# Kernel optimization log

Hardware: AMD Instinct MI355X
Metric: run time of the kernel (lower is better)

The kernel has to match this reference:

```python
import jax, jax.numpy as jnp
import numpy as np

N = 4096      # nodes
F_IN = 512    # nfeat
D = 64        # nhid per head
H = 8         # nheads
C = 16        # nclass
K = 2         # k hops
ALPHA = 0.2   # leakyrelu slope
BETA = 0.9    # hop decay
NEG = jnp.float32(-9e15)


def _lrelu(v):
    return jnp.where(v > 0, v, ALPHA * v)


def setup_inputs() -> dict:
    key = jax.random.key(0)
    ks = jax.random.split(key, 8)
    x = jax.random.normal(ks[0], (N, F_IN), jnp.float32)
    # k-hop neighbor masks (dense, sparse-ish occupancy); self-loops kept so no row is fully masked
    masks = jax.random.bernoulli(ks[1], 0.01, (K, N, N))
    masks = masks | jnp.eye(N, dtype=bool)[None]
    W = jax.random.normal(ks[2], (H, F_IN, D), jnp.float32) * 0.05
    a1 = jax.random.normal(ks[3], (H, D), jnp.float32) * 0.05
    a2 = jax.random.normal(ks[4], (H, D), jnp.float32) * 0.05
    W_out = jax.random.normal(ks[5], (H * D, C), jnp.float32) * 0.05
    a_out1 = jax.random.normal(ks[6], (C,), jnp.float32) * 0.05
    a_out2 = jax.random.normal(ks[7], (C,), jnp.float32) * 0.05
    return dict(x=x, masks=masks, W=W, a1=a1, a2=a2, W_out=W_out, a_out1=a_out1, a_out2=a_out2)


def reference(x, masks, W, a1, a2, W_out, a_out1, a_out2):
    # ---- multi-head k-hop GAT layers (concat=True) ----
    Wh = jnp.einsum('nf,hfd->hnd', x, W)                      # [H,N,D]
    f1 = jnp.einsum('hnd,hd->hn', Wh, a1)                     # source term
    f2 = jnp.einsum('hnd,hd->hn', Wh, a2)                     # target term
    e = _lrelu(f1[:, :, None] + f2[:, None, :])               # [H,N,N]
    h = jnp.zeros_like(Wh)
    for hop in range(K):                                      # fixed small k
        att = jax.nn.softmax(jnp.where(masks[hop][None], e, NEG), axis=-1)
        h = h + (BETA ** hop) * jnp.einsum('hnm,hmd->hnd', att, Wh)
    h = jax.nn.elu(h)                                         # concat=True applies elu
    x2 = jnp.transpose(h, (1, 0, 2)).reshape(N, H * D)        # head concat

    # ---- output k-hop attention layer (concat=False) ----
    Who = x2 @ W_out                                          # [N,C]
    e2 = _lrelu((Who @ a_out1)[:, None] + (Who @ a_out2)[None, :])  # [N,N]
    out = jnp.zeros_like(Who)
    for hop in range(K):
        att = jax.nn.softmax(jnp.where(masks[hop], e2, NEG), axis=-1)
        out = out + (BETA ** hop) * (att @ Who)
    out = jax.nn.elu(out)
    return jax.nn.log_softmax(out, axis=1)
```

## Files before the change

kernel.cpp:

```cpp
#include <hip/hip_runtime.h>
#include <cstdint>

#define NN 4096
#define FIN 512
#define DD 64
#define HH 8
#define CC 16
#define KHOP 2
#define ALPHA 0.2f
#define BETA 0.9f

typedef __attribute__((ext_vector_type(8))) short short8;
typedef __attribute__((ext_vector_type(4))) float floatx4;

static __device__ __forceinline__ uint16_t f2bf(float f) {
    uint32_t u = __float_as_uint(f);
    u += 0x7FFFu + ((u >> 16) & 1u);
    return (uint16_t)(u >> 16);
}

static __device__ __forceinline__ uint32_t nz_nib(uint32_t x) {
    uint32_t zero80 = (x - 0x01010101u) & ~x & 0x80808080u;
    uint32_t nz80 = zero80 ^ 0x80808080u;
    return ((nz80 >> 7) * 0x01020408u) >> 24;
}

__global__ __launch_bounds__(256) void bits_prep(const uint32_t* __restrict__ mraw,
                                                 uint64_t* __restrict__ bits,
                                                 const float* __restrict__ W,
                                                 uint16_t* __restrict__ Wt) {
    const int tid = threadIdx.x;
    if (blockIdx.x >= 1024) {
        const int b = blockIdx.x - 1024;
        const int h = b >> 3, kt = b & 7;
        __shared__ float tile[64][65];
        {
            const int kr = tid >> 4, d4 = (tid & 15) * 4;
#pragma unroll
            for (int r = 0; r < 4; ++r) {
                const int k = kr + r * 16;
                float4 v = *(const float4*)&W[((size_t)h * FIN + kt * 64 + k) * DD + d4];
                tile[k][d4 + 0] = v.x; tile[k][d4 + 1] = v.y;
                tile[k][d4 + 2] = v.z; tile[k][d4 + 3] = v.w;
            }
        }
        __syncthreads();
        const int d = tid >> 2, kb = (tid & 3) * 16;
        uint16_t tmp[16];
#pragma unroll
        for (int i = 0; i < 16; ++i) tmp[i] = f2bf(tile[kb + i][d]);
        uint4 o0, o1;
        o0.x = tmp[0] | ((uint32_t)tmp[1] << 16);  o0.y = tmp[2] | ((uint32_t)tmp[3] << 16);
        o0.z = tmp[4] | ((uint32_t)tmp[5] << 16);  o0.w = tmp[6] | ((uint32_t)tmp[7] << 16);
        o1.x = tmp[8] | ((uint32_t)tmp[9] << 16);  o1.y = tmp[10] | ((uint32_t)tmp[11] << 16);
        o1.z = tmp[12] | ((uint32_t)tmp[13] << 16); o1.w = tmp[14] | ((uint32_t)tmp[15] << 16);
        uint16_t* dst = Wt + ((size_t)h * DD + d) * FIN + kt * 64 + kb;
        *(uint4*)dst = o0;
        *(uint4*)(dst + 8) = o1;
        return;
    }
    const int totalWords = KHOP * NN * (NN / 64);
    __shared__ int sflag;
    if (tid == 0) sflag = 1;
    __syncthreads();
    bool ok = true;
    for (int i = tid; i < 4096; i += 256) {
        uint32_t w = mraw[i];
        if (!(w == 0u || w == 1u || w == 0x3F800000u)) ok = false;
    }
    if (!ok) sflag = 0;
    __syncthreads();
    const int flag = sflag;

    const int wave_id = (blockIdx.x * 256 + tid) >> 6;
    const int lane = tid & 63;

    if (!flag) {
        const uint8_t* m8 = (const uint8_t*)mraw;
        const uint8_t* base = m8 + (size_t)wave_id * 8192 + (size_t)lane * 16;
        uint4 v[8];
#pragma unroll
        for (int i = 0; i < 8; ++i)
            v[i] = *(const uint4*)(base + (size_t)i * 1024);
        const int idx = (lane & 15) * 4;
#pragma unroll
        for (int i = 0; i < 8; ++i) {
            uint32_t m16 = nz_nib(v[i].x) | (nz_nib(v[i].y) << 4) |
                           (nz_nib(v[i].z) << 8) | (nz_nib(v[i].w) << 12);
            uint32_t u0 = (uint32_t)__shfl((int)m16, idx);
            uint32_t u1 = (uint32_t)__shfl((int)m16, idx + 1);
            uint32_t u2 = (uint32_t)__shfl((int)m16, idx + 2);
            uint32_t u3 = (uint32_t)__shfl((int)m16, idx + 3);
            if (lane < 16) {
                uint64_t wrd = (uint64_t)((u0 & 0xFFFFu) | (u1 << 16)) |
                               ((uint64_t)((u2 & 0xFFFFu) | (u3 << 16)) << 32);
                bits[(size_t)wave_id * 128 + i * 16 + lane] = wrd;
            }
        }
    } else {
        const int w0b = wave_id * 128;
        for (int w0 = w0b; w0 < w0b + 128 && w0 < totalWords; w0 += 8) {
            uint32_t v[8];
#pragma unroll
            for (int i = 0; i < 8; ++i)
                v[i] = mraw[(size_t)(w0 + i) * 64 + lane];
#pragma unroll
            for (int i = 0; i < 8; ++i) {
                unsigned long long b = __ballot(v[i] != 0u);
                if (lane == 0) bits[w0 + i] = b;
            }
        }
    }
}

__global__ __launch_bounds__(256) void wh_gemm(const float* __restrict__ x,
                                               const uint16_t* __restrict__ Wt,
                                               const float* __restrict__ a1,
                                               const float* __restrict__ a2,
                                               uint16_t* __restrict__ Whb,
                                               float* __restrict__ f1,
                                               float* __restrict__ f2) {
    const int h = blockIdx.y;
    const int n0 = blockIdx.x * 64;
    const int tid = threadIdx.x;
    const int wave = tid >> 6, lane = tid & 63;
    const int q = lane >> 4, r = lane & 15;
    __shared__ uint16_t xs[64 * 72];
    __shared__ uint16_t ws[64 * 72];
    floatx4 acc[4] = {floatx4{0,0,0,0}, floatx4{0,0,0,0}, floatx4{0,0,0,0}, floatx4{0,0,0,0}};

    for (int chunk = 0; chunk < 8; ++chunk) {
        const int fc = chunk * 64;
        {
            const int row = tid >> 4, c4 = (tid & 15) * 4;
#pragma unroll
            for (int rr = 0; rr < 4; ++rr) {
                const int n = row + rr * 16;
                float4 v = *(const float4*)&x[(size_t)(n0 + n) * FIN + fc + c4];
                ushort4 o;
                o.x = f2bf(v.x); o.y = f2bf(v.y); o.z = f2bf(v.z); o.w = f2bf(v.w);
                *(ushort4*)&xs[n * 72 + c4] = o;
            }
            const int d = tid >> 2, kb = (tid & 3) * 16;
            const uint16_t* src = Wt + ((size_t)h * DD + d) * FIN + fc + kb;
            uint4 w0 = *(const uint4*)src;
            uint4 w1 = *(const uint4*)(src + 8);
            *(uint4*)&ws[d * 72 + kb] = w0;
            *(uint4*)&ws[d * 72 + kb + 8] = w1;
        }
        __syncthreads();
        const int mrow = wave * 16 + r;
        short8 a0 = *(const short8*)&xs[mrow * 72 + q * 8];
        short8 a1f = *(const short8*)&xs[mrow * 72 + 32 + q * 8];
#pragma unroll
        for (int t = 0; t < 4; ++t) {
            short8 b0 = *(const short8*)&ws[(t * 16 + r) * 72 + q * 8];
            short8 b1 = *(const short8*)&ws[(t * 16 + r) * 72 + 32 + q * 8];
            acc[t] = __builtin_amdgcn_mfma_f32_16x16x32_bf16(a0, b0, acc[t], 0, 0, 0);
            acc[t] = __builtin_amdgcn_mfma_f32_16x16x32_bf16(a1f, b1, acc[t], 0, 0, 0);
        }
        __syncthreads();
    }

#pragma unroll
    for (int t = 0; t < 4; ++t) {
#pragma unroll
        for (int reg = 0; reg < 4; ++reg) {
            const int m = wave * 16 + q * 4 + reg;
            const int d = t * 16 + r;
            Whb[((size_t)h * NN + n0 + m) * DD + d] = f2bf(acc[t][reg]);
        }
    }
    float a1r[4], a2r[4];
#pragma unroll
    for (int t = 0; t < 4; ++t) {
        a1r[t] = a1[h * DD + t * 16 + r];
        a2r[t] = a2[h * DD + t * 16 + r];
    }
#pragma unroll
    for (int reg = 0; reg < 4; ++reg) {
        float p1 = 0.f, p2 = 0.f;
#pragma unroll
        for (int t = 0; t < 4; ++t) {
            p1 += acc[t][reg] * a1r[t];
            p2 += acc[t][reg] * a2r[t];
        }
#pragma unroll
        for (int off = 1; off < 16; off <<= 1) {
            p1 += __shfl_xor(p1, off);
            p2 += __shfl_xor(p2, off);
        }
        if (r == 0) {
            const int m = wave * 16 + q * 4 + reg;
            f1[h * NN + n0 + m] = p1;
            f2[h * NN + n0 + m] = p2;
        }
    }
}

__global__ __launch_bounds__(512) void attn1(const uint64_t* __restrict__ bits,
                                             const uint16_t* __restrict__ Whb,
                                             const float* __restrict__ f1,
                                             const float* __restrict__ f2,
                                             const float* __restrict__ Wout,
                                             const float* __restrict__ ao1,
                                             const float* __restrict__ ao2,
                                             float* __restrict__ Who,
                                             float* __restrict__ g1,
                                             float* __restrict__ g2) {
    const int n = blockIdx.x;
    const int tid = threadIdx.x;
    const int h = tid >> 6, lane = tid & 63;
    const int hl = lane & 31, uh = lane >> 5;
    __shared__ uint16_t nbr[KHOP][NN];
    __shared__ uint2 wm[HH][64];
    __shared__ float xrow[HH * DD];
    __shared__ float part[32][17];
    __shared__ int cnt[KHOP];
    if (h < KHOP) {
        const int hop = h;
        if (lane == 0) cnt[hop] = 0;
        uint64_t v = bits[((size_t)hop * NN + n) * 64 + lane];
        int c = __popcll(v);
        int base = 0;
        if (c) base = atomicAdd(&cnt[hop], c);
        int mb = lane * 64;
        while (v) {
            int j = __ffsll((unsigned long long)v) - 1;
            nbr[hop][base++] = (uint16_t)(mb + j);
            v &= v - 1;
        }
    }
    const float f1n = f1[h * NN + n];
    const float* __restrict__ f2h = f2 + h * NN;
    const uint16_t* __restrict__ hb = Whb + (size_t)h * NN * DD;
    const uint32_t dbyte = (uint32_t)hl * 4;
    __syncthreads();
    float res0 = 0.f, res1 = 0.f;
    for (int hop = 0; hop < KHOP; ++hop) {
        const int count = cnt[hop];
        const uint16_t* __restrict__ nb = nbr[hop];
        uint2* __restrict__ wmh = wm[h];
        float acc0 = 0.f, acc1 = 0.f, denp = 0.f;
        for (int b0 = 0; b0 < count; b0 += 64) {
            const int bs = min(64, count - b0);
            uint32_t wbits = 0u, moff = 0u;
            if (lane < bs) {
                int m = nb[b0 + lane];
                float e = f1n + f2h[m];
                e = (e > 0.f) ? e : ALPHA * e;
                float w = __expf(e);
                denp += w;
                wbits = __float_as_uint(w);
                moff = (uint32_t)m << 7;
            }
            wmh[lane] = make_uint2(wbits, moff);
            const int npair8 = ((((bs + 1) >> 1) + 7) & ~7);
            for (int c0 = 0; c0 < npair8; c0 += 8) {
                uint2 pw[8];
#pragma unroll
                for (int i = 0; i < 8; ++i)
                    pw[i] = wmh[2 * (c0 + i) + uh];
#pragma unroll
                for (int i = 0; i < 8; ++i) {
                    const uint32_t dv =
                        *(const uint32_t*)((const char*)hb + (pw[i].y + dbyte));
                    const float w = __uint_as_float(pw[i].x);
                    acc0 += w * __uint_as_float(dv << 16);
                    acc1 += w * __uint_as_float(dv & 0xFFFF0000u);
                }
            }
        }
        float den = denp;
#pragma unroll
        for (int off = 1; off < 64; off <<= 1) den += __shfl_xor(den, off);
        acc0 += __shfl_xor(acc0, 32);
        acc1 += __shfl_xor(acc1, 32);
        const float scale = ((hop == 0) ? 1.f : BETA) / den;
        res0 += scale * acc0;
        res1 += scale * acc1;
    }
    float v0 = (res0 > 0.f) ? res0 : (__expf(res0) - 1.f);
    float v1 = (res1 > 0.f) ? res1 : (__expf(res1) - 1.f);
    if (uh == 0) {
        xrow[h * DD + 2 * hl]     = v0;
        xrow[h * DD + 2 * hl + 1] = v1;
    }
    __syncthreads();
    {
        const int c = tid & 15, chunk = tid >> 4;
        float p = 0.f;
#pragma unroll
        for (int i = 0; i < 16; ++i)
            p += xrow[chunk * 16 + i] * Wout[(chunk * 16 + i) * CC + c];
        part[chunk][c] = p;
    }
    __syncthreads();
    if (tid < 16) {
        float s = 0.f;
#pragma unroll
        for (int k = 0; k < 32; ++k) s += part[k][tid];
        Who[n * CC + tid] = s;
        float p1 = s * ao1[tid];
        float p2 = s * ao2[tid];
#pragma unroll
        for (int off = 1; off < 16; off <<= 1) {
            p1 += __shfl_xor(p1, off);
            p2 += __shfl_xor(p2, off);
        }
        if (tid == 0) { g1[n] = p1; g2[n] = p2; }
    }
}

__global__ __launch_bounds__(256) void attn2(const uint64_t* __restrict__ bits,
                                             const float* __restrict__ Who,
                                             const float* __restrict__ g1,
                                             const float* __restrict__ g2,
                                             float* __restrict__ out) {
    const int wv = threadIdx.x >> 6;
    const int lane = threadIdx.x & 63;
    const int n = blockIdx.x * 4 + wv;
    __shared__ uint16_t nbr[4][NN];
    uint16_t* mynbr = nbr[wv];
    const float g1n = g1[n];
    const int c = lane & 15, s = lane >> 4;
    const uint32_t cbyte = (uint32_t)c * 4;
    float res = 0.f;
    for (int hop = 0; hop < KHOP; ++hop) {
        uint64_t v = bits[((size_t)hop * NN + n) * 64 + lane];
        int cpc = __popcll(v);
        int pref = cpc;
        for (int off = 1; off < 64; off <<= 1) {
            int t = __shfl_up(pref, off);
            if (lane >= off) pref += t;
        }
        int total = __shfl(pref, 63);
        int base = pref - cpc;
        int mb = lane * 64;
        while (v) {
            int j = __ffsll((unsigned long long)v) - 1;
            mynbr[base++] = (uint16_t)(mb + j);
            v &= v - 1;
        }
        float acc = 0.f, denp = 0.f;
        for (int b0 = 0; b0 < total; b0 += 64) {
            const int bs = min(64, total - b0);
            float w = 0.f; uint32_t moff = 0u;
            if (lane < bs) {
                int m = mynbr[b0 + lane];
                float e = g1n + g2[m];
                e = (e > 0.f) ? e : ALPHA * e;
                w = __expf(e);
                moff = (uint32_t)m << 6;
            }
            denp += w;
            const int nit = (((bs + 3) >> 2) + 1) & ~1;
#pragma unroll 2
            for (int i = 0; i < nit; ++i) {
                const int j = 4 * i + s;
                const float wj = __shfl(w, j);
                const uint32_t oj = (uint32_t)__shfl((int)moff, j);
                const float v2 = *(const float*)((const char*)Who + (oj + cbyte));
                acc += wj * v2;
            }
        }
        float den = denp;
#pragma unroll
        for (int off = 1; off < 64; off <<= 1) den += __shfl_xor(den, off);
        acc += __shfl_xor(acc, 16);
        acc += __shfl_xor(acc, 32);
        res += ((hop == 0) ? 1.f : BETA) * (acc / den);
    }
    float o = (res > 0.f) ? res : (__expf(res) - 1.f);
    float mx = o;
    for (int off = 1; off < 16; off <<= 1) mx = fmaxf(mx, __shfl_xor(mx, off));
    float ex = __expf(o - mx);
    float sum = ex;
    for (int off = 1; off < 16; off <<= 1) sum += __shfl_xor(sum, off);
    float r = o - mx - __logf(sum);
    if (lane < 16) out[n * CC + c] = r;
}

extern "C" void kernel_launch(void* const* d_in, const int* in_sizes, int n_in,
                              void* d_out, int out_size, void* d_ws, size_t ws_size,
                              hipStream_t stream) {
    const float* x    = (const float*)d_in[0];
    const void*  masks= d_in[1];
    const float* W    = (const float*)d_in[2];
    const float* a1   = (const float*)d_in[3];
    const float* a2   = (const float*)d_in[4];
    const float* Wout = (const float*)d_in[5];
    const float* ao1  = (const float*)d_in[6];
    const float* ao2  = (const float*)d_in[7];
    float* out = (float*)d_out;

    char* ws = (char*)d_ws;
    uint64_t* bits = (uint64_t*)ws;
    uint16_t* Whb  = (uint16_t*)(ws + (size_t)KHOP * NN * 64 * 8);
    float* f1  = (float*)(Whb + (size_t)HH * NN * DD);
    float* f2  = f1 + (size_t)HH * NN;
    float* Who = f2 + (size_t)HH * NN;
    float* g1  = Who + (size_t)NN * CC;
    float* g2  = g1 + NN;
    uint16_t* Wt = (uint16_t*)(g2 + NN);

    bits_prep<<<1024 + HH * (FIN / 64), 256, 0, stream>>>((const uint32_t*)masks, bits, W, Wt);
    wh_gemm<<<dim3(NN / 64, HH), 256, 0, stream>>>(x, Wt, a1, a2, Whb, f1, f2);
    attn1<<<NN, 512, 0, stream>>>(bits, Whb, f1, f2, Wout, ao1, ao2, Who, g1, g2);
    attn2<<<NN / 4, 256, 0, stream>>>(bits, Who, g1, g2, out);
    (void)in_sizes; (void)n_in; (void)out_size; (void)ws_size;
}
```

Measured before the change: 280.6 us.

## Pre-convert x to bf16 once and widen gather loads in attention kernels

Adds extra blocks to the prep kernel that convert x to bf16 once, so wh_gemm no longer re-reads and converts fp32 x for each of the 8 heads. attn1 now has each lane load 16 bytes (8 bf16 features) per neighbor, with 8 neighbors processed in parallel per wave, instead of 4-byte loads. attn2 likewise switches to float4 gathers with 16 neighbors per step. This cuts redundant global traffic and load instruction count, at the cost of more register use and a larger cross-lane reduction.

```diff
diff --git a/kernel.cpp b/kernel.cpp
--- a/kernel.cpp
+++ b/kernel.cpp
@@ -28,8 +28,30 @@
 __global__ __launch_bounds__(256) void bits_prep(const uint32_t* __restrict__ mraw,
                                                  uint64_t* __restrict__ bits,
                                                  const float* __restrict__ W,
-                                                 uint16_t* __restrict__ Wt) {
+                                                 uint16_t* __restrict__ Wt,
+                                                 const float* __restrict__ x,
+                                                 uint16_t* __restrict__ xb) {
     const int tid = threadIdx.x;
+    if (blockIdx.x >= 1088) {
+        const int b = blockIdx.x - 1088;
+        const size_t base = ((size_t)b * 256 + tid) * 16;
+        float4 v0 = *(const float4*)&x[base];
+        float4 v1 = *(const float4*)&x[base + 4];
+        float4 v2 = *(const float4*)&x[base + 8];
+        float4 v3 = *(const float4*)&x[base + 12];
+        uint4 o0, o1;
+        o0.x = f2bf(v0.x) | ((uint32_t)f2bf(v0.y) << 16);
+        o0.y = f2bf(v0.z) | ((uint32_t)f2bf(v0.w) << 16);
+        o0.z = f2bf(v1.x) | ((uint32_t)f2bf(v1.y) << 16);
+        o0.w = f2bf(v1.z) | ((uint32_t)f2bf(v1.w) << 16);
+        o1.x = f2bf(v2.x) | ((uint32_t)f2bf(v2.y) << 16);
+        o1.y = f2bf(v2.z) | ((uint32_t)f2bf(v2.w) << 16);
+        o1.z = f2bf(v3.x) | ((uint32_t)f2bf(v3.y) << 16);
+        o1.w = f2bf(v3.z) | ((uint32_t)f2bf(v3.w) << 16);
+        *(uint4*)&xb[base] = o0;
+        *(uint4*)&xb[base + 8] = o1;
+        return;
+    }
     if (blockIdx.x >= 1024) {
         const int b = blockIdx.x - 1024;
         const int h = b >> 3, kt = b & 7;
@@ -113,7 +135,7 @@
     }
 }
 
-__global__ __launch_bounds__(256) void wh_gemm(const float* __restrict__ x,
+__global__ __launch_bounds__(256) void wh_gemm(const uint16_t* __restrict__ xb,
                                                const uint16_t* __restrict__ Wt,
                                                const float* __restrict__ a1,
                                                const float* __restrict__ a2,
@@ -129,24 +151,16 @@
     __shared__ uint16_t ws[64 * 72];
     floatx4 acc[4] = {floatx4{0,0,0,0}, floatx4{0,0,0,0}, floatx4{0,0,0,0}, floatx4{0,0,0,0}};
 
+    const int srow = tid >> 2, c16 = (tid & 3) * 16;
     for (int chunk = 0; chunk < 8; ++chunk) {
         const int fc = chunk * 64;
         {
-            const int row = tid >> 4, c4 = (tid & 15) * 4;
-#pragma unroll
-            for (int rr = 0; rr < 4; ++rr) {
-                const int n = row + rr * 16;
-                float4 v = *(const float4*)&x[(size_t)(n0 + n) * FIN + fc + c4];
-                ushort4 o;
-                o.x = f2bf(v.x); o.y = f2bf(v.y); o.z = f2bf(v.z); o.w = f2bf(v.w);
-                *(ushort4*)&xs[n * 72 + c4] = o;
-            }
-            const int d = tid >> 2, kb = (tid & 3) * 16;
-            const uint16_t* src = Wt + ((size_t)h * DD + d) * FIN + fc + kb;
-            uint4 w0 = *(const uint4*)src;
-            uint4 w1 = *(const uint4*)(src + 8);
-            *(uint4*)&ws[d * 72 + kb] = w0;
-            *(uint4*)&ws[d * 72 + kb + 8] = w1;
+            const uint16_t* xsrc = xb + (size_t)(n0 + srow) * FIN + fc + c16;
+            *(uint4*)&xs[srow * 72 + c16]     = *(const uint4*)xsrc;
+            *(uint4*)&xs[srow * 72 + c16 + 8] = *(const uint4*)(xsrc + 8);
+            const uint16_t* wsrc = Wt + ((size_t)h * DD + srow) * FIN + fc + c16;
+            *(uint4*)&ws[srow * 72 + c16]     = *(const uint4*)wsrc;
+            *(uint4*)&ws[srow * 72 + c16 + 8] = *(const uint4*)(wsrc + 8);
         }
         __syncthreads();
         const int mrow = wave * 16 + r;
@@ -211,7 +225,9 @@
     const int n = blockIdx.x;
     const int tid = threadIdx.x;
     const int h = tid >> 6, lane = tid & 63;
-    const int hl = lane & 31, uh = lane >> 5;
+    const int ng = lane >> 3;
+    const int dl = lane & 7;
+    const uint32_t dby = (uint32_t)dl * 16;
     __shared__ uint16_t nbr[KHOP][NN];
     __shared__ uint2 wm[HH][64];
     __shared__ float xrow[HH * DD];
@@ -234,14 +250,14 @@
     const float f1n = f1[h * NN + n];
     const float* __restrict__ f2h = f2 + h * NN;
     const uint16_t* __restrict__ hb = Whb + (size_t)h * NN * DD;
-    const uint32_t dbyte = (uint32_t)hl * 4;
     __syncthreads();
-    float res0 = 0.f, res1 = 0.f;
+    float res[8] = {0.f,0.f,0.f,0.f,0.f,0.f,0.f,0.f};
     for (int hop = 0; hop < KHOP; ++hop) {
         const int count = cnt[hop];
         const uint16_t* __restrict__ nb = nbr[hop];
         uint2* __restrict__ wmh = wm[h];
-        float acc0 = 0.f, acc1 = 0.f, denp = 0.f;
+        float acc[8] = {0.f,0.f,0.f,0.f,0.f,0.f,0.f,0.f};
+        float denp = 0.f;
         for (int b0 = 0; b0 < count; b0 += 64) {
             const int bs = min(64, count - b0);
             uint32_t wbits = 0u, moff = 0u;
@@ -255,36 +271,50 @@
                 moff = (uint32_t)m << 7;
             }
             wmh[lane] = make_uint2(wbits, moff);
-            const int npair8 = ((((bs + 1) >> 1) + 7) & ~7);
-            for (int c0 = 0; c0 < npair8; c0 += 8) {
-                uint2 pw[8];
-#pragma unroll
-                for (int i = 0; i < 8; ++i)
-                    pw[i] = wmh[2 * (c0 + i) + uh];
-#pragma unroll
-                for (int i = 0; i < 8; ++i) {
-                    const uint32_t dv =
-                        *(const uint32_t*)((const char*)hb + (pw[i].y + dbyte));
-                    const float w = __uint_as_float(pw[i].x);
-                    acc0 += w * __uint_as_float(dv << 16);
-                    acc1 += w * __uint_as_float(dv & 0xFFFF0000u);
-                }
+            const int ngrp = (bs + 15) >> 4;
+            for (int g = 0; g < ngrp; ++g) {
+                const uint2 p0 = wmh[g * 16 + ng];
+                const uint2 p1 = wmh[g * 16 + 8 + ng];
+                const uint4 d0 = *(const uint4*)((const char*)hb + (p0.y + dby));
+                const uint4 d1 = *(const uint4*)((const char*)hb + (p1.y + dby));
+                const float w0 = __uint_as_float(p0.x);
+                const float w1 = __uint_as_float(p1.x);
+                acc[0] += w0 * __uint_as_float(d0.x << 16);
+                acc[1] += w0 * __uint_as_float(d0.x & 0xFFFF0000u);
+                acc[2] += w0 * __uint_as_float(d0.y << 16);
+                acc[3] += w0 * __uint_as_float(d0.y & 0xFFFF0000u);
+                acc[4] += w0 * __uint_as_float(d0.z << 16);
+                acc[5] += w0 * __uint_as_float(d0.z & 0xFFFF0000u);
+                acc[6] += w0 * __uint_as_float(d0.w << 16);
+                acc[7] += w0 * __uint_as_float(d0.w & 0xFFFF0000u);
+                acc[0] += w1 * __uint_as_float(d1.x << 16);
+                acc[1] += w1 * __uint_as_float(d1.x & 0xFFFF0000u);
+                acc[2] += w1 * __uint_as_float(d1.y << 16);
+                acc[3] += w1 * __uint_as_float(d1.y & 0xFFFF0000u);
+                acc[4] += w1 * __uint_as_float(d1.z << 16);
+                acc[5] += w1 * __uint_as_float(d1.z & 0xFFFF0000u);
+                acc[6] += w1 * __uint_as_float(d1.w << 16);
+                acc[7] += w1 * __uint_as_float(d1.w & 0xFFFF0000u);
             }
         }
         float den = denp;
 #pragma unroll
         for (int off = 1; off < 64; off <<= 1) den += __shfl_xor(den, off);
-        acc0 += __shfl_xor(acc0, 32);
-        acc1 += __shfl_xor(acc1, 32);
+#pragma unroll
+        for (int off = 8; off < 64; off <<= 1) {
+#pragma unroll
+            for (int d = 0; d < 8; ++d) acc[d] += __shfl_xor(acc[d], off);
+        }
         const float scale = ((hop == 0) ? 1.f : BETA) / den;
-        res0 += scale * acc0;
-        res1 += scale * acc1;
-    }
-    float v0 = (res0 > 0.f) ? res0 : (__expf(res0) - 1.f);
-    float v1 = (res1 > 0.f) ? res1 : (__expf(res1) - 1.f);
-    if (uh == 0) {
-        xrow[h * DD + 2 * hl]     = v0;
-        xrow[h * DD + 2 * hl + 1] = v1;
+#pragma unroll
+        for (int d = 0; d < 8; ++d) res[d] += scale * acc[d];
+    }
+    if (ng == 0) {
+#pragma unroll
+        for (int d = 0; d < 8; ++d) {
+            const float v = res[d];
+            xrow[h * DD + dl * 8 + d] = (v > 0.f) ? v : (__expf(v) - 1.f);
+        }
     }
     __syncthreads();
     {
@@ -323,9 +353,9 @@
     __shared__ uint16_t nbr[4][NN];
     uint16_t* mynbr = nbr[wv];
     const float g1n = g1[n];
-    const int c = lane & 15, s = lane >> 4;
-    const uint32_t cbyte = (uint32_t)c * 4;
-    float res = 0.f;
+    const int s4 = lane >> 2, cg = lane & 3;
+    const uint32_t cby = (uint32_t)cg * 16;
+    float res[4] = {0.f,0.f,0.f,0.f};
     for (int hop = 0; hop < KHOP; ++hop) {
         uint64_t v = bits[((size_t)hop * NN + n) * 64 + lane];
         int cpc = __popcll(v);
@@ -342,7 +372,8 @@
             mynbr[base++] = (uint16_t)(mb + j);
             v &= v - 1;
         }
-        float acc = 0.f, denp = 0.f;
+        float acc[4] = {0.f,0.f,0.f,0.f};
+        float denp = 0.f;
         for (int b0 = 0; b0 < total; b0 += 64) {
             const int bs = min(64, total - b0);
             float w = 0.f; uint32_t moff = 0u;
@@ -354,31 +385,48 @@
                 moff = (uint32_t)m << 6;
             }
             denp += w;
-            const int nit = (((bs + 3) >> 2) + 1) & ~1;
-#pragma unroll 2
-            for (int i = 0; i < nit; ++i) {
-                const int j = 4 * i + s;
+            const int nstep = (bs + 15) >> 4;
+            for (int i = 0; i < nstep; ++i) {
+                const int j = 16 * i + s4;
                 const float wj = __shfl(w, j);
                 const uint32_t oj = (uint32_t)__shfl((int)moff, j);
-                const float v2 = *(const float*)((const char*)Who + (oj + cbyte));
-                acc += wj * v2;
+                const float4 vv = *(const float4*)((const char*)Who + (oj + cby));
+                acc[0] += wj * vv.x;
+                acc[1] += wj * vv.y;
+                acc[2] += wj * vv.z;
+                acc[3] += wj * vv.w;
             }
         }
         float den = denp;
 #pragma unroll
         for (int off = 1; off < 64; off <<= 1) den += __shfl_xor(den, off);
-        acc += __shfl_xor(acc, 16);
-        acc += __shfl_xor(acc, 32);
-        res += ((hop == 0) ? 1.f : BETA) * (acc / den);
-    }
-    float o = (res > 0.f) ? res : (__expf(res) - 1.f);
-    float mx = o;
-    for (int off = 1; off < 16; off <<= 1) mx = fmaxf(mx, __shfl_xor(mx, off));
-    float ex = __expf(o - mx);
-    float sum = ex;
-    for (int off = 1; off < 16; off <<= 1) sum += __shfl_xor(sum, off);
-    float r = o - mx - __logf(sum);
-    if (lane < 16) out[n * CC + c] = r;
+#pragma unroll
+        for (int off = 4; off < 64; off <<= 1) {
+#pragma unroll
+            for (int d = 0; d < 4; ++d) acc[d] += __shfl_xor(acc[d], off);
+        }
+        const float sc = ((hop == 0) ? 1.f : BETA) / den;
+#pragma unroll
+        for (int d = 0; d < 4; ++d) res[d] += sc * acc[d];
+    }
+    float o[4];
+#pragma unroll
+    for (int d = 0; d < 4; ++d) o[d] = (res[d] > 0.f) ? res[d] : (__expf(res[d]) - 1.f);
+    float mx = fmaxf(fmaxf(o[0], o[1]), fmaxf(o[2], o[3]));
+#pragma unroll
+    for (int off = 1; off < 4; off <<= 1) mx = fmaxf(mx, __shfl_xor(mx, off));
+    float s = 0.f;
+#pragma unroll
+    for (int d = 0; d < 4; ++d) s += __expf(o[d] - mx);
+#pragma unroll
+    for (int off = 1; off < 4; off <<= 1) s += __shfl_xor(s, off);
+    const float lg = __logf(s);
+    if (s4 == 0) {
+        float4 r;
+        r.x = o[0] - mx - lg; r.y = o[1] - mx - lg;
+        r.z = o[2] - mx - lg; r.w = o[3] - mx - lg;
+        *(float4*)&out[(size_t)n * CC + cg * 4] = r;
+    }
 }
 
 extern "C" void kernel_launch(void* const* d_in, const int* in_sizes, int n_in,
@@ -403,9 +451,10 @@
     float* g1  = Who + (size_t)NN * CC;
     float* g2  = g1 + NN;
     uint16_t* Wt = (uint16_t*)(g2 + NN);
-
-    bits_prep<<<1024 + HH * (FIN / 64), 256, 0, stream>>>((const uint32_t*)masks, bits, W, Wt);
-    wh_gemm<<<dim3(NN / 64, HH), 256, 0, stream>>>(x, Wt, a1, a2, Whb, f1, f2);
+    uint16_t* xb = Wt + (size_t)HH * DD * FIN;
+
+    bits_prep<<<1088 + 512, 256, 0, stream>>>((const uint32_t*)masks, bits, W, Wt, x, xb);
+    wh_gemm<<<dim3(NN / 64, HH), 256, 0, stream>>>(xb, Wt, a1, a2, Whb, f1, f2);
     attn1<<<NN, 512, 0, stream>>>(bits, Whb, f1, f2, Wout, ao1, ao2, Who, g1, g2);
     attn2<<<NN / 4, 256, 0, stream>>>(bits, Who, g1, g2, out);
     (void)in_sizes; (void)n_in; (void)out_size; (void)ws_size;
```

Measured after the change: 281.5 us. About the same (+0.3%).
